# Kernel tuning notes

Hardware: AMD Instinct MI355X
Metric: run time of the kernel (lower is better)

Reference implementation:

```python
import jax, jax.numpy as jnp
import numpy as np

B, S, D = 4, 2048, 1024
H, DH = 16, 64  # num_heads, output_dim per head
NEG = -1e9


def setup_inputs() -> dict:
    key = jax.random.key(0)
    ks = jax.random.split(key, 12)
    inp = {
        "query": jax.random.normal(ks[0], (B, S, D), dtype=jnp.float32),
        "key": jax.random.normal(ks[1], (B, S, D), dtype=jnp.float32),
        "value": jax.random.normal(ks[2], (B, S, D), dtype=jnp.float32),
        "mask": jax.random.randint(ks[3], (B, S, S), 0, 2, dtype=jnp.int32),
    }
    sc = 1.0 / np.sqrt(D)
    sco = 1.0 / np.sqrt(H * DH)
    # stacked per-head projection weights: [H, D, DH] (nn.Linear applies x @ W.T; we store W.T directly)
    inp["Wq"] = jax.random.uniform(ks[4], (H, D, DH), jnp.float32, -sc, sc)
    inp["bq"] = jax.random.uniform(ks[5], (H, DH), jnp.float32, -sc, sc)
    inp["Wk"] = jax.random.uniform(ks[6], (H, D, DH), jnp.float32, -sc, sc)
    inp["bk"] = jax.random.uniform(ks[7], (H, DH), jnp.float32, -sc, sc)
    inp["Wv"] = jax.random.uniform(ks[8], (H, D, DH), jnp.float32, -sc, sc)
    inp["bv"] = jax.random.uniform(ks[9], (H, DH), jnp.float32, -sc, sc)
    inp["Wo"] = jax.random.uniform(ks[10], (H * DH, DH), jnp.float32, -sco, sco)
    inp["bo"] = jax.random.uniform(ks[11], (DH,), jnp.float32, -sco, sco)
    return inp


def reference(query, key, value, mask, Wq, bq, Wk, bk, Wv, bv, Wo, bo):
    # batched per-head projections: [B,S,D] x [H,D,DH] -> [B,H,S,DH]
    q = jnp.einsum("bsd,hde->bhse", query, Wq) + bq[None, :, None, :]
    k = jnp.einsum("bsd,hde->bhse", key, Wk) + bk[None, :, None, :]
    v = jnp.einsum("bsd,hde->bhse", value, Wv) + bv[None, :, None, :]
    # NOTE: original module does NOT scale by 1/sqrt(DH)
    scores = jnp.einsum("bhse,bhte->bhst", q, k)  # [B,H,S,S]
    scores = jnp.where(mask[:, None, :, :] == 0, NEG, scores)
    attn = jax.nn.softmax(scores, axis=-1)
    out = jnp.einsum("bhst,bhte->bhse", attn, v)  # [B,H,S,DH]
    # concat heads (head order matches torch.cat over loop): [B,S,H*DH]
    cat = out.transpose(0, 2, 1, 3).reshape(query.shape[0], query.shape[1], -1)
    return cat @ Wo + bo
```

## Files before the change

### kernel.cpp

```cpp
#include <hip/hip_runtime.h>
#include <hip/hip_bf16.h>

typedef __attribute__((ext_vector_type(8))) short bf16x8;
typedef __attribute__((ext_vector_type(4))) float f32x4;
typedef unsigned int u32;
typedef unsigned short u16;
typedef unsigned long long u64;


__device__ __forceinline__ void gload_lds16(const void* g, void* l) {
    __builtin_amdgcn_global_load_lds(
        (const __attribute__((address_space(1))) void*)g,
        (__attribute__((address_space(3))) void*)l, 16, 0, 0);
}

__device__ __forceinline__ u16 f2bf(float f) {
    u32 u = __builtin_bit_cast(u32, f);
    u32 r = u + 0x7fffu + ((u >> 16) & 1u);
    return (u16)(r >> 16);
}

__global__ void k_cvt(const float* __restrict__ in, u16* __restrict__ out, int n) {
    int i = (blockIdx.x * blockDim.x + threadIdx.x) * 4;
    int stride = gridDim.x * blockDim.x * 4;
    for (; i < n; i += stride) {
        float4 v = *(const float4*)(in + i);
        ushort4 o = make_ushort4(f2bf(v.x), f2bf(v.y), f2bf(v.z), f2bf(v.w));
        *(ushort4*)(out + i) = o;
    }
}

__global__ void k_pack_w(const float* __restrict__ W, u16* __restrict__ Wt) {
    int i = blockIdx.x * 256 + threadIdx.x;
    int h = i >> 16;
    int r = i & 65535;
    int k = r >> 6, e = r & 63;
    Wt[(size_t)(h * 64 + e) * 1024 + k] = f2bf(W[i]);
}

__global__ void k_pack_wo(const float* __restrict__ W, u16* __restrict__ Wt) {
    int i = blockIdx.x * 256 + threadIdx.x;
    int k = i >> 6, e = i & 63;
    Wt[(size_t)e * 1024 + k] = f2bf(W[i]);
}

__global__ void k_pack_mask(const int* __restrict__ mask, u32* __restrict__ bits) {
    size_t i = (size_t)blockIdx.x * 256 + threadIdx.x;
    int m = mask[i];
    u64 bal = __ballot(m != 0);
    if ((threadIdx.x & 63) == 0) *(u64*)(bits + (i >> 5)) = bal;
}

__global__ __launch_bounds__(256) void k_proj(
    const u16* __restrict__ A, const u16* __restrict__ Bt,
    const float* __restrict__ bias, u16* __restrict__ out, int mode, float oscale)
{
    __shared__ char smem[16384];
    const int tid = threadIdx.x, lane = tid & 63, w = tid >> 6;
    const int wr = w >> 1, wc = w & 1;
    const int fr = lane & 15, fq = lane >> 4;

    const int flat = blockIdx.y * 8 + blockIdx.x;
    const int xcd = flat & 7, idx = flat >> 3;
    const int xb = idx >> 3;
    const int yb = xcd * 8 + (idx & 7);
    const int m0 = yb * 128, n0 = xb * 128;

    const int arow = w * 32 + (lane >> 2);
    const int aseg = (lane & 3) * 8;

    f32x4 acc[4][4] = {};

    for (int kt = 0; kt < 1024; kt += 32) {
#pragma unroll
        for (int t = 0; t < 2; ++t) {
            gload_lds16(A + (size_t)(m0 + arow + t * 16) * 1024 + kt + aseg,
                        smem + w * 2048 + t * 1024);
            gload_lds16(Bt + (size_t)(n0 + arow + t * 16) * 1024 + kt + aseg,
                        smem + 8192 + w * 2048 + t * 1024);
        }
        __syncthreads();
        bf16x8 af[4], bfv[4];
#pragma unroll
        for (int m = 0; m < 4; ++m)
            af[m] = *(const bf16x8*)(smem + (wr * 64 + m * 16 + fr) * 64 + fq * 16);
#pragma unroll
        for (int n = 0; n < 4; ++n)
            bfv[n] = *(const bf16x8*)(smem + 8192 + (wc * 64 + n * 16 + fr) * 64 + fq * 16);
#pragma unroll
        for (int m = 0; m < 4; ++m)
#pragma unroll
            for (int n = 0; n < 4; ++n)
                acc[m][n] = __builtin_amdgcn_mfma_f32_16x16x32_bf16(af[m], bfv[n], acc[m][n], 0, 0, 0);
        __syncthreads();
    }

#pragma unroll
    for (int m = 0; m < 4; ++m) {
#pragma unroll
        for (int n = 0; n < 4; ++n) {
            int col = n0 + wc * 64 + n * 16 + fr;
            float bvv = bias[col];
            int h = col >> 6, e = col & 63;
            if (mode == 0) {
#pragma unroll
                for (int j = 0; j < 4; ++j) {
                    int row = m0 + wr * 64 + m * 16 + fq * 4 + j;
                    int bb = row >> 11, s = row & 2047;
                    out[((size_t)(bb * 16 + h) * 2048 + s) * 64 + e] = f2bf((acc[m][n][j] + bvv) * oscale);
                }
            } else {
                int row = m0 + wr * 64 + m * 16 + fq * 4;
                int bb = row >> 11, s = row & 2047;
                ushort4 o = make_ushort4(f2bf(acc[m][n][0] + bvv), f2bf(acc[m][n][1] + bvv),
                                         f2bf(acc[m][n][2] + bvv), f2bf(acc[m][n][3] + bvv));
                *(ushort4*)(out + ((size_t)(bb * 16 + h) * 64 + e) * 2048 + s) = o;
            }
        }
    }
}

__global__ __launch_bounds__(256) void k_attn(
    const u16* __restrict__ Qg_, const u16* __restrict__ Kg_,
    const u16* __restrict__ Vg_, const u32* __restrict__ mbits,
    u16* __restrict__ O)
{
    __shared__ char smem[49152];
    const int tid = threadIdx.x, lane = tid & 63, w = tid >> 6;
    const int fr = lane & 15, fq = lane >> 4;
    char* Ps = smem + 32768 + w * 4096;

    const int bid = blockIdx.x;
    const int wg = (bid & 7) * 128 + (bid >> 3);
    const int bh = wg >> 4, qt = wg & 15;
    const int b = bh >> 4;
    const int q0 = qt * 128, wq0 = w * 32;

    const u16* Qg = Qg_ + (size_t)bh * 2048 * 64;
    const u16* Kg = Kg_ + (size_t)bh * 2048 * 64;
    const u16* Vg = Vg_ + (size_t)bh * 64 * 2048;

    bf16x8 qf[2][2];
#pragma unroll
    for (int m = 0; m < 2; ++m)
#pragma unroll
        for (int ks = 0; ks < 2; ++ks)
            qf[m][ks] = *(const bf16x8*)(Qg + (size_t)(q0 + wq0 + m * 16 + fr) * 64 + ks * 32 + fq * 8);

    f32x4 acc[2][4] = {};
    f32x4 acc_l[2] = {};

    const bf16x8 onesv = {(short)0x3F80, (short)0x3F80, (short)0x3F80, (short)0x3F80,
                          (short)0x3F80, (short)0x3F80, (short)0x3F80, (short)0x3F80};

    const int srow = w * 16 + (lane >> 3);
    const int sseg0 = lane & 7;

#pragma unroll
    for (int tt = 0; tt < 2; ++tt) {
        int row = srow + tt * 8;
        int seg = sseg0 ^ (row & 7);
        gload_lds16(Kg + (size_t)row * 64 + seg * 8, smem + w * 2048 + tt * 1024);
        gload_lds16(Vg + (size_t)row * 2048 + seg * 8, smem + 8192 + w * 2048 + tt * 1024);
    }
    __syncthreads();

    const u32* mrow_base = mbits + ((size_t)b * 2048 + q0 + wq0) * 64;

    for (int t = 0; t < 32; ++t) {
        const int cur = t & 1;
        char* Ks = smem + cur * 16384;
        char* Vs = Ks + 8192;

        if (t + 1 < 32) {
            char* Kn = smem + (cur ^ 1) * 16384;
            int kvn = (t + 1) * 64;
#pragma unroll
            for (int tt = 0; tt < 2; ++tt) {
                int row = srow + tt * 8;
                int seg = sseg0 ^ (row & 7);
                gload_lds16(Kg + (size_t)(kvn + row) * 64 + seg * 8, Kn + w * 2048 + tt * 1024);
                gload_lds16(Vg + (size_t)row * 2048 + kvn + seg * 8, Kn + 8192 + w * 2048 + tt * 1024);
            }
        }

        u64 mw[2][4];
#pragma unroll
        for (int m = 0; m < 2; ++m)
#pragma unroll
            for (int j = 0; j < 4; ++j)
                mw[m][j] = *(const u64*)(mrow_base + (size_t)(m * 16 + fq * 4 + j) * 64 + t * 2);

        f32x4 sc[2][4] = {};
#pragma unroll
        for (int ks = 0; ks < 2; ++ks) {
#pragma unroll
            for (int n = 0; n < 4; ++n) {
                int row = n * 16 + fr;
                int c16 = (ks * 4 + fq) ^ (row & 7);
                bf16x8 kf = *(const bf16x8*)(Ks + row * 128 + c16 * 16);
#pragma unroll
                for (int m = 0; m < 2; ++m)
                    sc[m][n] = __builtin_amdgcn_mfma_f32_16x16x32_bf16(qf[m][ks], kf, sc[m][n], 0, 0, 0);
            }
        }

#pragma unroll
        for (int m = 0; m < 2; ++m) {
#pragma unroll
            for (int j = 0; j < 4; ++j) {
                u32 lo = (u32)mw[m][j], hi = (u32)(mw[m][j] >> 32);
                int ql = m * 16 + fq * 4 + j;
#pragma unroll
                for (int n = 0; n < 4; ++n) {
                    u32 word = (n < 2) ? lo : hi;
                    u32 bit = (word >> (((n & 1) << 4) + fr)) & 1u;
                    float e = __builtin_amdgcn_exp2f(sc[m][n][j]);
                    float p = bit ? e : 0.f;
                    int kvl = n * 16 + fr;
                    *(u16*)(Ps + ql * 128 + (((kvl >> 3) ^ (ql & 7)) << 4) + (kvl & 7) * 2) = f2bf(p);
                }
            }
        }

#pragma unroll
        for (int ks = 0; ks < 2; ++ks) {
            bf16x8 pf[2];
#pragma unroll
            for (int m = 0; m < 2; ++m) {
                int row = m * 16 + fr;
                pf[m] = *(const bf16x8*)(Ps + row * 128 + (((ks * 4 + fq) ^ (row & 7)) << 4));
            }
#pragma unroll
            for (int m = 0; m < 2; ++m)
                acc_l[m] = __builtin_amdgcn_mfma_f32_16x16x32_bf16(pf[m], onesv, acc_l[m], 0, 0, 0);
#pragma unroll
            for (int ne = 0; ne < 4; ++ne) {
                int vrow = ne * 16 + fr;
                int c16 = (ks * 4 + fq) ^ (vrow & 7);
                bf16x8 vf = *(const bf16x8*)(Vs + vrow * 128 + c16 * 16);
#pragma unroll
                for (int m = 0; m < 2; ++m)
                    acc[m][ne] = __builtin_amdgcn_mfma_f32_16x16x32_bf16(pf[m], vf, acc[m][ne], 0, 0, 0);
            }
        }
        __syncthreads();
    }

    const int h = bh & 15;
#pragma unroll
    for (int m = 0; m < 2; ++m)
#pragma unroll
        for (int j = 0; j < 4; ++j) {
            float inv = 1.0f / acc_l[m][j];
            int sq = q0 + wq0 + m * 16 + fq * 4 + j;
#pragma unroll
            for (int ne = 0; ne < 4; ++ne)
                O[((size_t)b * 2048 + sq) * 1024 + h * 64 + ne * 16 + fr] =
                    f2bf(acc[m][ne][j] * inv);
        }
}

__global__ __launch_bounds__(256) void k_oproj(
    const u16* __restrict__ A, const u16* __restrict__ Bt,
    const float* __restrict__ bo, float* __restrict__ out)
{
    __shared__ char smem[8192 + 4096];
    const int tid = threadIdx.x, lane = tid & 63, w = tid >> 6;
    const int fr = lane & 15, fq = lane >> 4;
    const int m0 = blockIdx.x * 128;

    const int arow = w * 32 + (lane >> 2);
    const int aseg = (lane & 3) * 8;
    const int brow = w * 16 + (lane >> 2);

    f32x4 acc[2][4] = {};

    for (int kt = 0; kt < 1024; kt += 32) {
#pragma unroll
        for (int t = 0; t < 2; ++t)
            gload_lds16(A + (size_t)(m0 + arow + t * 16) * 1024 + kt + aseg,
                        smem + w * 2048 + t * 1024);
        gload_lds16(Bt + (size_t)brow * 1024 + kt + aseg, smem + 8192 + w * 1024);
        __syncthreads();
        bf16x8 af[2], bfv[4];
#pragma unroll
        for (int m = 0; m < 2; ++m)
            af[m] = *(const bf16x8*)(smem + (w * 32 + m * 16 + fr) * 64 + fq * 16);
#pragma unroll
        for (int n = 0; n < 4; ++n)
            bfv[n] = *(const bf16x8*)(smem + 8192 + (n * 16 + fr) * 64 + fq * 16);
#pragma unroll
        for (int m = 0; m < 2; ++m)
#pragma unroll
            for (int n = 0; n < 4; ++n)
                acc[m][n] = __builtin_amdgcn_mfma_f32_16x16x32_bf16(af[m], bfv[n], acc[m][n], 0, 0, 0);
        __syncthreads();
    }

#pragma unroll
    for (int m = 0; m < 2; ++m)
#pragma unroll
        for (int n = 0; n < 4; ++n) {
            float bb = bo[n * 16 + fr];
#pragma unroll
            for (int j = 0; j < 4; ++j)
                out[(size_t)(m0 + w * 32 + m * 16 + fq * 4 + j) * 64 + n * 16 + fr] =
                    acc[m][n][j] + bb;
        }
}

extern "C" void kernel_launch(void* const* d_in, const int* in_sizes, int n_in,
                              void* d_out, int out_size, void* d_ws, size_t ws_size,
                              hipStream_t stream) {
    const float* query = (const float*)d_in[0];
    const float* key   = (const float*)d_in[1];
    const float* value = (const float*)d_in[2];
    const int*   mask  = (const int*)d_in[3];
    const float* Wq = (const float*)d_in[4];
    const float* bq = (const float*)d_in[5];
    const float* Wk = (const float*)d_in[6];
    const float* bk = (const float*)d_in[7];
    const float* Wv = (const float*)d_in[8];
    const float* bv = (const float*)d_in[9];
    const float* Wo = (const float*)d_in[10];
    const float* bo = (const float*)d_in[11];
    float* out = (float*)d_out;

    char* ws = (char*)d_ws;
    size_t off = 0;
    auto alloc = [&](size_t bytes) {
        size_t o = off;
        off += (bytes + 255) & ~(size_t)255;
        return o;
    };
    u16* xq  = (u16*)(ws + alloc(16777216));
    u16* xk  = (u16*)(ws + alloc(16777216));
    u16* xv  = (u16*)(ws + alloc(16777216));
    u16* wtq = (u16*)(ws + alloc(2097152));
    u16* wtk = (u16*)(ws + alloc(2097152));
    u16* wtv = (u16*)(ws + alloc(2097152));
    u16* wot = (u16*)(ws + alloc(131072));
    u16* qh  = (u16*)(ws + alloc(16777216));
    u16* kh  = (u16*)(ws + alloc(16777216));
    u16* vt  = (u16*)(ws + alloc(16777216));
    u32* mb  = (u32*)(ws + alloc(2097152));
    u16* attno = xq;

    k_cvt<<<2048, 256, 0, stream>>>(query, xq, 8388608);
    k_cvt<<<2048, 256, 0, stream>>>(key,   xk, 8388608);
    k_cvt<<<2048, 256, 0, stream>>>(value, xv, 8388608);
    k_pack_w<<<4096, 256, 0, stream>>>(Wq, wtq);
    k_pack_w<<<4096, 256, 0, stream>>>(Wk, wtk);
    k_pack_w<<<4096, 256, 0, stream>>>(Wv, wtv);
    k_pack_wo<<<256, 256, 0, stream>>>(Wo, wot);
    k_pack_mask<<<65536, 256, 0, stream>>>(mask, mb);

    k_proj<<<dim3(8, 64), 256, 0, stream>>>(xq, wtq, bq, qh, 0, 1.44269504088896f);
    k_proj<<<dim3(8, 64), 256, 0, stream>>>(xk, wtk, bk, kh, 0, 1.0f);
    k_proj<<<dim3(8, 64), 256, 0, stream>>>(xv, wtv, bv, vt, 1, 1.0f);

    k_attn<<<1024, 256, 0, stream>>>(qh, kh, vt, mb, attno);

    k_oproj<<<64, 256, 0, stream>>>(attno, wot, bo, out);
}
```

Baseline: 324.4 us.

## Widen attention blocks to 512 threads sharing K/V tiles, add MFMA priority hints

The attention kernel now launches 512-thread blocks of 8 waves covering 256 queries, so each K/V tile staged in LDS serves twice as many query rows. Global K/V traffic per query drops, and each thread issues one load per tile instead of two. Mask words are now loaded just before use instead of being prefetched ahead of the QK MFMAs, and s_setprio hints are placed around the MFMA phases. LDS grows to 64KB per block and there are fewer blocks, which may reduce occupancy and expose mask-load latency.

```diff
diff --git a/kernel.cpp b/kernel.cpp
--- a/kernel.cpp
+++ b/kernel.cpp
@@ -6,6 +6,8 @@
 typedef unsigned int u32;
 typedef unsigned short u16;
 typedef unsigned long long u64;
+
+typedef bf16x8 __attribute__((may_alias)) bf16x8_ma;
 
 
 __device__ __forceinline__ void gload_lds16(const void* g, void* l) {
@@ -83,10 +85,10 @@
         bf16x8 af[4], bfv[4];
 #pragma unroll
         for (int m = 0; m < 4; ++m)
-            af[m] = *(const bf16x8*)(smem + (wr * 64 + m * 16 + fr) * 64 + fq * 16);
+            af[m] = *(const bf16x8_ma*)(smem + (wr * 64 + m * 16 + fr) * 64 + fq * 16);
 #pragma unroll
         for (int n = 0; n < 4; ++n)
-            bfv[n] = *(const bf16x8*)(smem + 8192 + (wc * 64 + n * 16 + fr) * 64 + fq * 16);
+            bfv[n] = *(const bf16x8_ma*)(smem + 8192 + (wc * 64 + n * 16 + fr) * 64 + fq * 16);
 #pragma unroll
         for (int m = 0; m < 4; ++m)
 #pragma unroll
@@ -120,21 +122,21 @@
     }
 }
 
-__global__ __launch_bounds__(256) void k_attn(
+__global__ __launch_bounds__(512, 4) void k_attn(
     const u16* __restrict__ Qg_, const u16* __restrict__ Kg_,
     const u16* __restrict__ Vg_, const u32* __restrict__ mbits,
     u16* __restrict__ O)
 {
-    __shared__ char smem[49152];
+    __shared__ char smem[65536];
     const int tid = threadIdx.x, lane = tid & 63, w = tid >> 6;
     const int fr = lane & 15, fq = lane >> 4;
     char* Ps = smem + 32768 + w * 4096;
 
     const int bid = blockIdx.x;
-    const int wg = (bid & 7) * 128 + (bid >> 3);
-    const int bh = wg >> 4, qt = wg & 15;
+    const int wg = (bid & 7) * 64 + (bid >> 3);
+    const int bh = wg >> 3, qt = wg & 7;
     const int b = bh >> 4;
-    const int q0 = qt * 128, wq0 = w * 32;
+    const int qw = qt * 256 + w * 32;
 
     const u16* Qg = Qg_ + (size_t)bh * 2048 * 64;
     const u16* Kg = Kg_ + (size_t)bh * 2048 * 64;
@@ -145,7 +147,7 @@
     for (int m = 0; m < 2; ++m)
 #pragma unroll
         for (int ks = 0; ks < 2; ++ks)
-            qf[m][ks] = *(const bf16x8*)(Qg + (size_t)(q0 + wq0 + m * 16 + fr) * 64 + ks * 32 + fq * 8);
+            qf[m][ks] = *(const bf16x8_ma*)(Qg + (size_t)(qw + m * 16 + fr) * 64 + ks * 32 + fq * 8);
 
     f32x4 acc[2][4] = {};
     f32x4 acc_l[2] = {};
@@ -153,83 +155,69 @@
     const bf16x8 onesv = {(short)0x3F80, (short)0x3F80, (short)0x3F80, (short)0x3F80,
                           (short)0x3F80, (short)0x3F80, (short)0x3F80, (short)0x3F80};
 
-    const int srow = w * 16 + (lane >> 3);
-    const int sseg0 = lane & 7;
-
-#pragma unroll
-    for (int tt = 0; tt < 2; ++tt) {
-        int row = srow + tt * 8;
-        int seg = sseg0 ^ (row & 7);
-        gload_lds16(Kg + (size_t)row * 64 + seg * 8, smem + w * 2048 + tt * 1024);
-        gload_lds16(Vg + (size_t)row * 2048 + seg * 8, smem + 8192 + w * 2048 + tt * 1024);
-    }
+    const int srow = w * 8 + (lane >> 3);
+    const int sseg = (lane & 7) ^ (srow & 7);
+
+    gload_lds16(Kg + (size_t)srow * 64 + sseg * 8, smem + w * 1024);
+    gload_lds16(Vg + (size_t)srow * 2048 + sseg * 8, smem + 8192 + w * 1024);
     __syncthreads();
 
-    const u32* mrow_base = mbits + ((size_t)b * 2048 + q0 + wq0) * 64;
+    const u32* mq = mbits + ((size_t)b * 2048 + qw) * 64;
 
     for (int t = 0; t < 32; ++t) {
-        const int cur = t & 1;
-        char* Ks = smem + cur * 16384;
+        char* Ks = smem + (t & 1) * 16384;
         char* Vs = Ks + 8192;
 
         if (t + 1 < 32) {
-            char* Kn = smem + (cur ^ 1) * 16384;
+            char* Kn = smem + ((t + 1) & 1) * 16384;
             int kvn = (t + 1) * 64;
-#pragma unroll
-            for (int tt = 0; tt < 2; ++tt) {
-                int row = srow + tt * 8;
-                int seg = sseg0 ^ (row & 7);
-                gload_lds16(Kg + (size_t)(kvn + row) * 64 + seg * 8, Kn + w * 2048 + tt * 1024);
-                gload_lds16(Vg + (size_t)row * 2048 + kvn + seg * 8, Kn + 8192 + w * 2048 + tt * 1024);
-            }
-        }
-
-        u64 mw[2][4];
-#pragma unroll
-        for (int m = 0; m < 2; ++m)
-#pragma unroll
-            for (int j = 0; j < 4; ++j)
-                mw[m][j] = *(const u64*)(mrow_base + (size_t)(m * 16 + fq * 4 + j) * 64 + t * 2);
+            gload_lds16(Kg + (size_t)(kvn + srow) * 64 + sseg * 8, Kn + w * 1024);
+            gload_lds16(Vg + (size_t)srow * 2048 + kvn + sseg * 8, Kn + 8192 + w * 1024);
+        }
 
         f32x4 sc[2][4] = {};
+        __builtin_amdgcn_s_setprio(1);
 #pragma unroll
         for (int ks = 0; ks < 2; ++ks) {
 #pragma unroll
             for (int n = 0; n < 4; ++n) {
                 int row = n * 16 + fr;
-                int c16 = (ks * 4 + fq) ^ (row & 7);
-                bf16x8 kf = *(const bf16x8*)(Ks + row * 128 + c16 * 16);
+                bf16x8 kf = *(const bf16x8_ma*)(Ks + row * 128 + (((ks * 4 + fq) ^ (row & 7)) << 4));
 #pragma unroll
                 for (int m = 0; m < 2; ++m)
                     sc[m][n] = __builtin_amdgcn_mfma_f32_16x16x32_bf16(qf[m][ks], kf, sc[m][n], 0, 0, 0);
             }
         }
+        __builtin_amdgcn_s_setprio(0);
 
 #pragma unroll
         for (int m = 0; m < 2; ++m) {
 #pragma unroll
             for (int j = 0; j < 4; ++j) {
-                u32 lo = (u32)mw[m][j], hi = (u32)(mw[m][j] >> 32);
                 int ql = m * 16 + fq * 4 + j;
+                u64 mw = *(const u64*)(mq + (size_t)ql * 64 + t * 2);
+                u32 lo = (u32)mw, hi = (u32)(mw >> 32);
 #pragma unroll
                 for (int n = 0; n < 4; ++n) {
+                    int kvl = n * 16 + fr;
                     u32 word = (n < 2) ? lo : hi;
-                    u32 bit = (word >> (((n & 1) << 4) + fr)) & 1u;
+                    u32 bit = (word >> (kvl & 31)) & 1u;
                     float e = __builtin_amdgcn_exp2f(sc[m][n][j]);
                     float p = bit ? e : 0.f;
-                    int kvl = n * 16 + fr;
                     *(u16*)(Ps + ql * 128 + (((kvl >> 3) ^ (ql & 7)) << 4) + (kvl & 7) * 2) = f2bf(p);
                 }
             }
         }
-
+        asm volatile("" ::: "memory");
+
+        __builtin_amdgcn_s_setprio(1);
 #pragma unroll
         for (int ks = 0; ks < 2; ++ks) {
             bf16x8 pf[2];
 #pragma unroll
             for (int m = 0; m < 2; ++m) {
                 int row = m * 16 + fr;
-                pf[m] = *(const bf16x8*)(Ps + row * 128 + (((ks * 4 + fq) ^ (row & 7)) << 4));
+                pf[m] = *(const bf16x8_ma*)(Ps + row * 128 + (((ks * 4 + fq) ^ (row & 7)) << 4));
             }
 #pragma unroll
             for (int m = 0; m < 2; ++m)
@@ -237,13 +225,13 @@
 #pragma unroll
             for (int ne = 0; ne < 4; ++ne) {
                 int vrow = ne * 16 + fr;
-                int c16 = (ks * 4 + fq) ^ (vrow & 7);
-                bf16x8 vf = *(const bf16x8*)(Vs + vrow * 128 + c16 * 16);
+                bf16x8 vf = *(const bf16x8_ma*)(Vs + vrow * 128 + (((ks * 4 + fq) ^ (vrow & 7)) << 4));
 #pragma unroll
                 for (int m = 0; m < 2; ++m)
                     acc[m][ne] = __builtin_amdgcn_mfma_f32_16x16x32_bf16(pf[m], vf, acc[m][ne], 0, 0, 0);
             }
         }
+        __builtin_amdgcn_s_setprio(0);
         __syncthreads();
     }
 
@@ -253,7 +241,7 @@
 #pragma unroll
         for (int j = 0; j < 4; ++j) {
             float inv = 1.0f / acc_l[m][j];
-            int sq = q0 + wq0 + m * 16 + fq * 4 + j;
+            int sq = qw + m * 16 + fq * 4 + j;
 #pragma unroll
             for (int ne = 0; ne < 4; ++ne)
                 O[((size_t)b * 2048 + sq) * 1024 + h * 64 + ne * 16 + fr] =
@@ -286,10 +274,10 @@
         bf16x8 af[2], bfv[4];
 #pragma unroll
         for (int m = 0; m < 2; ++m)
-            af[m] = *(const bf16x8*)(smem + (w * 32 + m * 16 + fr) * 64 + fq * 16);
+            af[m] = *(const bf16x8_ma*)(smem + (w * 32 + m * 16 + fr) * 64 + fq * 16);
 #pragma unroll
         for (int n = 0; n < 4; ++n)
-            bfv[n] = *(const bf16x8*)(smem + 8192 + (n * 16 + fr) * 64 + fq * 16);
+            bfv[n] = *(const bf16x8_ma*)(smem + 8192 + (n * 16 + fr) * 64 + fq * 16);
 #pragma unroll
         for (int m = 0; m < 2; ++m)
 #pragma unroll
@@ -360,7 +348,7 @@
     k_proj<<<dim3(8, 64), 256, 0, stream>>>(xk, wtk, bk, kh, 0, 1.0f);
     k_proj<<<dim3(8, 64), 256, 0, stream>>>(xv, wtv, bv, vt, 1, 1.0f);
 
-    k_attn<<<1024, 256, 0, stream>>>(qh, kh, vt, mb, attno);
+    k_attn<<<512, 512, 0, stream>>>(qh, kh, vt, mb, attno);
 
     k_oproj<<<64, 256, 0, stream>>>(attno, wot, bo, out);
 }
```

New measurement: 495.3 us. +52.7%, slower.
